# Kernel tuning notes

Hardware: AMD Instinct MI355X
Metric: run time of the kernel (lower is better)

The kernel has to match this reference:

```python
import jax, jax.numpy as jnp
import numpy as np

N, E, F_IN, H, C = 50000, 800000, 128, 4, 64
NEG_SLOPE = 0.2
LN_EPS = 1e-5


def setup_inputs() -> dict:
    key = jax.random.key(0)
    ks = jax.random.split(key, 8)
    s = 0.05
    return {
        "x": jax.random.normal(ks[0], (N, F_IN), jnp.float32),
        "edge_index": jax.random.randint(ks[1], (2, E), 0, N, jnp.int64).astype(jnp.int32),
        "Wl": jax.random.normal(ks[2], (F_IN, H * C), jnp.float32) * s,
        "bl": jnp.zeros((H * C,), jnp.float32),
        "Wr": jax.random.normal(ks[3], (F_IN, H * C), jnp.float32) * s,
        "br": jnp.zeros((H * C,), jnp.float32),
        "att": jax.random.normal(ks[4], (H, C), jnp.float32) * s,
        "bias_out": jnp.zeros((H * C,), jnp.float32),
        "Wproj": jax.random.normal(ks[5], (H * C, C), jnp.float32) * s,
        "ln_w": jnp.ones((C,), jnp.float32),
        "ln_b": jnp.zeros((C,), jnp.float32),
        "Wres": jax.random.normal(ks[6], (F_IN, C), jnp.float32) * s,
    }


def reference(x, edge_index, Wl, bl, Wr, br, att, bias_out, Wproj, ln_w, ln_b, Wres):
    n = x.shape[0]
    # add self loops (GATv2Conv add_self_loops=True)
    loop = jnp.arange(n, dtype=edge_index.dtype)
    src = jnp.concatenate([edge_index[0], loop])
    dst = jnp.concatenate([edge_index[1], loop])

    xl = (x @ Wl + bl).reshape(n, H, C)  # source-side transform
    xr = (x @ Wr + br).reshape(n, H, C)  # target-side transform

    # GATv2 edge scores: a^T LeakyReLU(xl_j + xr_i)
    m = xl[src] + xr[dst]                              # [Etot, H, C]
    e = jnp.einsum('ehc,hc->eh', jax.nn.leaky_relu(m, NEG_SLOPE), att)

    # segment softmax over incoming edges per destination node
    emax = jax.ops.segment_max(e, dst, num_segments=n)  # every node has a self loop
    ex = jnp.exp(e - emax[dst])
    denom = jax.ops.segment_sum(ex, dst, num_segments=n)
    alpha = ex / denom[dst]                             # [Etot, H]

    # scatter-aggregate messages, concat heads, output bias
    msg = xl[src] * alpha[:, :, None]                   # [Etot, H, C]
    out = jax.ops.segment_sum(msg, dst, num_segments=n).reshape(n, H * C) + bias_out

    # proj -> layernorm -> GELU -> (+ residual); dropout inactive in eval
    out = out @ Wproj                                   # [N, C]
    mu = out.mean(-1, keepdims=True)
    var = jnp.mean(jnp.square(out - mu), -1, keepdims=True)
    out = (out - mu) * jax.lax.rsqrt(var + LN_EPS) * ln_w + ln_b
    out = jax.nn.gelu(out, approximate=False)
    return out + x @ Wres
```

## Files before the change

### kernel.cpp

```cpp
#include <hip/hip_runtime.h>
#include <math.h>

#define NEG_SLOPE 0.2f
#define LN_EPS 1e-5f
#define HC 256
#define NHEAD 4
#define CDIM 64
#define FIN 128
#define CAP 96

typedef short bf16x8 __attribute__((ext_vector_type(8)));
typedef float f32x4  __attribute__((ext_vector_type(4)));

__device__ inline unsigned short f2bf(float f) {
    unsigned u = __builtin_bit_cast(unsigned, f);
    return (unsigned short)((u + 0x7FFFu + ((u >> 16) & 1u)) >> 16);
}
__device__ inline float bf2f(unsigned short s) {
    return __builtin_bit_cast(float, (unsigned)s << 16);
}
__device__ inline void unpack8(const uint4 u, float* f) {
    f[0] = __builtin_bit_cast(float, u.x << 16);
    f[1] = __builtin_bit_cast(float, u.x & 0xffff0000u);
    f[2] = __builtin_bit_cast(float, u.y << 16);
    f[3] = __builtin_bit_cast(float, u.y & 0xffff0000u);
    f[4] = __builtin_bit_cast(float, u.z << 16);
    f[5] = __builtin_bit_cast(float, u.z & 0xffff0000u);
    f[6] = __builtin_bit_cast(float, u.w << 16);
    f[7] = __builtin_bit_cast(float, u.w & 0xffff0000u);
}

__global__ __launch_bounds__(256) void k_setup(
    const float* __restrict__ x,
    const float* __restrict__ Wl, const float* __restrict__ Wr,
    const float* __restrict__ Wproj, const float* __restrict__ Wres,
    const float* __restrict__ bias_out, const float* __restrict__ att,
    const int* __restrict__ ei,
    ushort* __restrict__ xb,
    ushort* __restrict__ wlb, ushort* __restrict__ wrb,
    ushort* __restrict__ wpj, ushort* __restrict__ wrs,
    float* __restrict__ bpj, float* __restrict__ att_s,
    int* __restrict__ cnt, int* __restrict__ bucket,
    int nb_sc, int nb_cvt, int E, int n_nodes)
{
    const int t = threadIdx.x;
    const int b = blockIdx.x;

    if (b < nb_sc) {
        const int gid = b * 256 + t;
        if (gid < E) {
            const int s = ei[gid];
            const int d = ei[E + gid];
            const int slot = atomicAdd(&cnt[d], 1);
            __builtin_nontemporal_store(s, &bucket[d * CAP + slot]);
        }
    } else if (b < nb_sc + nb_cvt) {
        const long i = ((long)(b - nb_sc) * 256 + t) * 4;
        const float4 v = *reinterpret_cast<const float4*>(&x[i]);
        ushort4 o;
        o.x = f2bf(v.x); o.y = f2bf(v.y); o.z = f2bf(v.z); o.w = f2bf(v.w);
        *reinterpret_cast<ushort4*>(&xb[i]) = o;
    } else if (b < nb_sc + nb_cvt + 224) {
        const int gid = (b - nb_sc - nb_cvt) * 256 + t;
        if (gid < 32768) {
            const int idx = gid;
            const int j = idx & 7, n = (idx >> 3) & 255, q = idx >> 11;
            const int k = (q >> 2) * 32 + (q & 3) * 8 + j;
            wlb[idx] = f2bf(Wl[k * HC + n]);
            wrb[idx] = f2bf(Wr[k * HC + n]);
        } else if (gid < 49152) {
            const int idx = gid - 32768;
            const int j = idx & 7, n = (idx >> 3) & 63, q = idx >> 9;
            const int k = (q >> 2) * 32 + (q & 3) * 8 + j;
            wpj[idx] = f2bf(Wproj[k * CDIM + n]);
        } else {
            const int idx = gid - 49152;
            const int j = idx & 7, n = (idx >> 3) & 63, q = idx >> 9;
            const int k = (q >> 2) * 32 + (q & 3) * 8 + j;
            wrs[idx] = f2bf(Wres[k * CDIM + n]);
        }
    } else {
        att_s[t] = att[t] * 1.44269504088896f;
        __shared__ float part[4][CDIM];
        const int col = t & 63, q = t >> 6;
        float s = 0.f;
        for (int k = q * 64; k < q * 64 + 64; ++k)
            s += bias_out[k] * Wproj[k * CDIM + col];
        part[q][col] = s;
        __syncthreads();
        if (q == 0)
            bpj[col] = part[0][col] + part[1][col] + part[2][col] + part[3][col];
    }
}

__global__ __launch_bounds__(256) void k_linear_mfma(
    const ushort* __restrict__ xb,
    const ushort* __restrict__ wlb, const ushort* __restrict__ wrb,
    const float* __restrict__ bl, const float* __restrict__ br,
    ushort* __restrict__ xl, ushort* __restrict__ xr, int n_nodes)
{
    const int wid = blockIdx.x * 4 + (threadIdx.x >> 6);
    const int lane = threadIdx.x & 63;
    const int ntiles = n_nodes >> 4;
    if (wid >= ntiles * 2) return;
    const int side = wid & 1;
    const int tile = wid >> 1;

    const ushort* __restrict__ wb   = side ? wrb : wlb;
    const float*  __restrict__ bias = side ? br : bl;
    ushort*       __restrict__ outp = side ? xr : xl;

    const int m  = lane & 15;
    const int kb = lane >> 4;
    const long arow = ((long)tile * 16 + m) * FIN;

    f32x4 acc[16];
#pragma unroll
    for (int f = 0; f < 16; ++f) acc[f] = (f32x4){0.f, 0.f, 0.f, 0.f};

    for (int ks = 0; ks < 4; ++ks) {
        const bf16x8 xf = *reinterpret_cast<const bf16x8*>(&xb[arow + ks * 32 + kb * 8]);
        const ushort* __restrict__ wq = wb + (size_t)((ks * 4 + kb) * HC) * 8;
#pragma unroll
        for (int f = 0; f < 16; ++f) {
            const bf16x8 wf = *reinterpret_cast<const bf16x8*>(&wq[(f * 16 + m) * 8]);
            acc[f] = __builtin_amdgcn_mfma_f32_16x16x32_bf16(wf, xf, acc[f], 0, 0, 0);
        }
    }
    const long obase = ((long)tile * 16 + m) * HC;
#pragma unroll
    for (int f = 0; f < 16; ++f) {
        const int ch = f * 16 + kb * 4;
        const float4 bi = *reinterpret_cast<const float4*>(&bias[ch]);
        ushort4 o;
        o.x = f2bf(acc[f][0] + bi.x);
        o.y = f2bf(acc[f][1] + bi.y);
        o.z = f2bf(acc[f][2] + bi.z);
        o.w = f2bf(acc[f][3] + bi.w);
        *reinterpret_cast<ushort4*>(&outp[obase + ch]) = o;
    }
}

__global__ __launch_bounds__(256) void k_gat_gather(
    const int* __restrict__ cnt, const int* __restrict__ bucket,
    const ushort* __restrict__ xl, const ushort* __restrict__ xr,
    const float* __restrict__ att_s,
    ushort* __restrict__ agg, int n_nodes)
{
    const int node = blockIdx.x * 4 + (threadIdx.x >> 6);
    const int lane = threadIdx.x & 63;
    if (node >= n_nodes) return;

    const int cn = cnt[node];
    const int half = lane >> 5;
    const unsigned ch = (unsigned)(lane & 31) * 8;

    float xrv[8], atv[8];
    unpack8(*reinterpret_cast<const uint4*>(&xr[(unsigned)node * HC + ch]), xrv);
    const float4 a0 = *reinterpret_cast<const float4*>(&att_s[ch]);
    const float4 a1 = *reinterpret_cast<const float4*>(&att_s[ch + 4]);
    atv[0] = a0.x; atv[1] = a0.y; atv[2] = a0.z; atv[3] = a0.w;
    atv[4] = a1.x; atv[5] = a1.y; atv[6] = a1.z; atv[7] = a1.w;

    float cs[8];
    unpack8(*reinterpret_cast<const uint4*>(&xl[(unsigned)node * HC + ch]), cs);
    float ps = 0.f;
#pragma unroll
    for (int j = 0; j < 8; ++j) {
        float m = cs[j] + xrv[j];
        m = fmaxf(m, NEG_SLOPE * m);
        ps += m * atv[j];
    }
    ps += __shfl_xor(ps, 1);
    ps += __shfl_xor(ps, 2);
    ps += __shfl_xor(ps, 4);
    float es;
    asm("v_exp_f32 %0, %1" : "=v"(es) : "v"(ps));
    es = (half == 0) ? es : 0.f;
    float den = es;
    float ac[8];
#pragma unroll
    for (int j = 0; j < 8; ++j) ac[j] = es * cs[j];

    if (cn > 0) {
        const int beg = node * CAP;
        const int end = beg + cn;
        const int last = end - 1;

        const int i0 = bucket[min(beg + half, last)];
        const int i1 = bucket[min(beg + 2 + half, last)];
        const int i2 = bucket[min(beg + 4 + half, last)];
        const int i3 = bucket[min(beg + 6 + half, last)];
        int ip = bucket[min(beg + 8 + half, last)];
        int iq = bucket[min(beg + 10 + half, last)];
        uint4 d0 = *reinterpret_cast<const uint4*>(&xl[((unsigned)i0 << 8) + ch]);
        uint4 d1 = *reinterpret_cast<const uint4*>(&xl[((unsigned)i1 << 8) + ch]);
        uint4 d2 = *reinterpret_cast<const uint4*>(&xl[((unsigned)i2 << 8) + ch]);
        uint4 d3 = *reinterpret_cast<const uint4*>(&xl[((unsigned)i3 << 8) + ch]);

        for (int k = beg; k < end; k += 2) {
            const uint4 cu = d0;
            d0 = d1; d1 = d2; d2 = d3;
            d3 = *reinterpret_cast<const uint4*>(&xl[((unsigned)ip << 8) + ch]);
            ip = iq;
            iq = bucket[min(k + 12 + half, last)];

            float c[8];
            unpack8(cu, c);
            float p = 0.f;
#pragma unroll
            for (int j = 0; j < 8; ++j) {
                float m = c[j] + xrv[j];
                m = fmaxf(m, NEG_SLOPE * m);
                p += m * atv[j];
            }
            p += __shfl_xor(p, 1);
            p += __shfl_xor(p, 2);
            p += __shfl_xor(p, 4);

            float e;
            asm("v_exp_f32 %0, %1" : "=v"(e) : "v"(p));
            e = (k + half < end) ? e : 0.f;
            den += e;
#pragma unroll
            for (int j = 0; j < 8; ++j) ac[j] += e * c[j];
        }
    }

    den += __shfl_xor(den, 32);
#pragma unroll
    for (int j = 0; j < 8; ++j) ac[j] += __shfl_xor(ac[j], 32);

    if (lane < 32) {
        const float inv = 1.f / den;
        uint4 o;
        o.x = ((unsigned)f2bf(ac[1] * inv) << 16) | f2bf(ac[0] * inv);
        o.y = ((unsigned)f2bf(ac[3] * inv) << 16) | f2bf(ac[2] * inv);
        o.z = ((unsigned)f2bf(ac[5] * inv) << 16) | f2bf(ac[4] * inv);
        o.w = ((unsigned)f2bf(ac[7] * inv) << 16) | f2bf(ac[6] * inv);
        *reinterpret_cast<uint4*>(&agg[(unsigned)node * HC + ch]) = o;
    }
}

__global__ __launch_bounds__(256) void k_post_mfma(
    const ushort* __restrict__ aggb, const ushort* __restrict__ xb,
    const ushort* __restrict__ wpj, const ushort* __restrict__ wrs,
    const float* __restrict__ bpj,
    const float* __restrict__ ln_w, const float* __restrict__ ln_b,
    float* __restrict__ out, int n_nodes)
{
    const int wid = blockIdx.x * 4 + (threadIdx.x >> 6);
    const int lane = threadIdx.x & 63;
    const int ntiles = n_nodes >> 4;
    if (wid >= ntiles) return;

    const int m  = lane & 15;
    const int kb = lane >> 4;
    const long node = (long)wid * 16 + m;
    const long gbase = node * HC;
    const long xbase = node * FIN;

    f32x4 ap[4], ar[4];
#pragma unroll
    for (int f = 0; f < 4; ++f) {
        ap[f] = (f32x4){0.f, 0.f, 0.f, 0.f};
        ar[f] = (f32x4){0.f, 0.f, 0.f, 0.f};
    }

    for (int ks = 0; ks < 8; ++ks) {
        const bf16x8 af = *reinterpret_cast<const bf16x8*>(&aggb[gbase + ks * 32 + kb * 8]);
        const ushort* __restrict__ wq = wpj + (size_t)((ks * 4 + kb) * CDIM) * 8;
#pragma unroll
        for (int f = 0; f < 4; ++f) {
            const bf16x8 wf = *reinterpret_cast<const bf16x8*>(&wq[(f * 16 + m) * 8]);
            ap[f] = __builtin_amdgcn_mfma_f32_16x16x32_bf16(wf, af, ap[f], 0, 0, 0);
        }
    }
    for (int ks = 0; ks < 4; ++ks) {
        const bf16x8 af = *reinterpret_cast<const bf16x8*>(&xb[xbase + ks * 32 + kb * 8]);
        const ushort* __restrict__ wq = wrs + (size_t)((ks * 4 + kb) * CDIM) * 8;
#pragma unroll
        for (int f = 0; f < 4; ++f) {
            const bf16x8 wf = *reinterpret_cast<const bf16x8*>(&wq[(f * 16 + m) * 8]);
            ar[f] = __builtin_amdgcn_mfma_f32_16x16x32_bf16(wf, af, ar[f], 0, 0, 0);
        }
    }

    float p[4][4];
#pragma unroll
    for (int f = 0; f < 4; ++f) {
        const float4 bp = *reinterpret_cast<const float4*>(&bpj[f * 16 + kb * 4]);
#pragma unroll
        for (int j = 0; j < 4; ++j) p[f][j] = ap[f][j] + ((const float*)&bp)[j];
    }

    float s1 = 0.f;
#pragma unroll
    for (int f = 0; f < 4; ++f)
#pragma unroll
        for (int j = 0; j < 4; ++j) s1 += p[f][j];
    s1 += __shfl_xor(s1, 16); s1 += __shfl_xor(s1, 32);
    const float mu = s1 * (1.f / 64.f);

    float s2 = 0.f;
#pragma unroll
    for (int f = 0; f < 4; ++f)
#pragma unroll
        for (int j = 0; j < 4; ++j) {
            const float d = p[f][j] - mu;
            s2 += d * d;
        }
    s2 += __shfl_xor(s2, 16); s2 += __shfl_xor(s2, 32);
    const float rs = rsqrtf(s2 * (1.f / 64.f) + LN_EPS);

#pragma unroll
    for (int f = 0; f < 4; ++f) {
        const int ch = f * 16 + kb * 4;
        const float4 lw = *reinterpret_cast<const float4*>(&ln_w[ch]);
        const float4 lb = *reinterpret_cast<const float4*>(&ln_b[ch]);
        float4 ov;
#pragma unroll
        for (int j = 0; j < 4; ++j) {
            const float v = (p[f][j] - mu) * rs * ((const float*)&lw)[j] + ((const float*)&lb)[j];
            const float g = 0.5f * v * (1.f + erff(v * 0.70710678118654752f));
            ((float*)&ov)[j] = g + ar[f][j];
        }
        *reinterpret_cast<float4*>(&out[node * CDIM + ch]) = ov;
    }
}

extern "C" void kernel_launch(void* const* d_in, const int* in_sizes, int n_in,
                              void* d_out, int out_size, void* d_ws, size_t ws_size,
                              hipStream_t stream)
{
    const float* x        = (const float*)d_in[0];
    const int*   ei       = (const int*)  d_in[1];
    const float* Wl       = (const float*)d_in[2];
    const float* bl       = (const float*)d_in[3];
    const float* Wr       = (const float*)d_in[4];
    const float* br       = (const float*)d_in[5];
    const float* att      = (const float*)d_in[6];
    const float* bias_out = (const float*)d_in[7];
    const float* Wproj    = (const float*)d_in[8];
    const float* ln_w     = (const float*)d_in[9];
    const float* ln_b     = (const float*)d_in[10];
    const float* Wres     = (const float*)d_in[11];
    float* out = (float*)d_out;

    const int N = in_sizes[0] / FIN;
    const int E = in_sizes[1] / 2;
    const int ntiles = N >> 4;

    ushort* us = (ushort*)d_ws;
    size_t uo = 0;
    ushort* xl_bf  = us + uo; uo += (size_t)N * HC;
    ushort* xr_bf  = us + uo; uo += (size_t)N * HC;
    ushort* agg_bf = us + uo; uo += (size_t)N * HC;
    ushort* x_bf   = us + uo; uo += (size_t)N * FIN;
    ushort* wlb    = us + uo; uo += 32768;
    ushort* wrb    = us + uo; uo += 32768;
    ushort* wpj    = us + uo; uo += 16384;
    ushort* wrs    = us + uo; uo += 8192;
    float* bpj   = (float*)(us + uo);
    float* att_s = bpj + CDIM;
    int* cnt    = (int*)(att_s + HC);
    int* bucket = cnt + N;

    hipMemsetAsync(cnt, 0, (size_t)N * sizeof(int), stream);

    const int nb_sc  = (E + 255) / 256;
    const int nb_cvt = (N * FIN / 4 + 255) / 256;
    k_setup<<<nb_sc + nb_cvt + 224 + 1, 256, 0, stream>>>(
        x, Wl, Wr, Wproj, Wres, bias_out, att, ei,
        x_bf, wlb, wrb, wpj, wrs, bpj, att_s, cnt, bucket,
        nb_sc, nb_cvt, E, N);

    k_linear_mfma<<<(2 * ntiles + 3) / 4, 256, 0, stream>>>(
        x_bf, wlb, wrb, bl, br, xl_bf, xr_bf, N);

    k_gat_gather<<<(N + 3) / 4, 256, 0, stream>>>(
        cnt, bucket, xl_bf, xr_bf, att_s, agg_bf, N);

    k_post_mfma<<<(ntiles + 3) / 4, 256, 0, stream>>>(
        agg_bf, x_bf, wpj, wrs, bpj, ln_w, ln_b, out, N);
}
```

Before: 252.8 us.

## Fuse edge bucketing and x conversion into linear MFMA kernel, pad counters

Splits setup into a small weight-prep kernel and a combined kernel that runs edge bucketing blocks alongside the linear MFMA blocks. The linear blocks now read fp32 x directly and convert it to bf16 in registers, with one side writing x_bf for the later post kernel. This removes the separate x conversion pass and one launch boundary. Per-node counters are padded to a 16-int stride to spread the atomics across cache lines, at the cost of a larger memset and more counter memory.

```diff
diff --git a/kernel.cpp b/kernel.cpp
--- a/kernel.cpp
+++ b/kernel.cpp
@@ -8,6 +8,7 @@
 #define CDIM 64
 #define FIN 128
 #define CAP 96
+#define CSTRIDE 16
 
 typedef short bf16x8 __attribute__((ext_vector_type(8)));
 typedef float f32x4  __attribute__((ext_vector_type(4)));
@@ -30,38 +31,18 @@
     f[7] = __builtin_bit_cast(float, u.w & 0xffff0000u);
 }
 
-__global__ __launch_bounds__(256) void k_setup(
-    const float* __restrict__ x,
+__global__ __launch_bounds__(256) void k_prep(
     const float* __restrict__ Wl, const float* __restrict__ Wr,
     const float* __restrict__ Wproj, const float* __restrict__ Wres,
     const float* __restrict__ bias_out, const float* __restrict__ att,
-    const int* __restrict__ ei,
-    ushort* __restrict__ xb,
     ushort* __restrict__ wlb, ushort* __restrict__ wrb,
     ushort* __restrict__ wpj, ushort* __restrict__ wrs,
-    float* __restrict__ bpj, float* __restrict__ att_s,
-    int* __restrict__ cnt, int* __restrict__ bucket,
-    int nb_sc, int nb_cvt, int E, int n_nodes)
+    float* __restrict__ bpj, float* __restrict__ att_s)
 {
     const int t = threadIdx.x;
     const int b = blockIdx.x;
-
-    if (b < nb_sc) {
+    if (b < 224) {
         const int gid = b * 256 + t;
-        if (gid < E) {
-            const int s = ei[gid];
-            const int d = ei[E + gid];
-            const int slot = atomicAdd(&cnt[d], 1);
-            __builtin_nontemporal_store(s, &bucket[d * CAP + slot]);
-        }
-    } else if (b < nb_sc + nb_cvt) {
-        const long i = ((long)(b - nb_sc) * 256 + t) * 4;
-        const float4 v = *reinterpret_cast<const float4*>(&x[i]);
-        ushort4 o;
-        o.x = f2bf(v.x); o.y = f2bf(v.y); o.z = f2bf(v.z); o.w = f2bf(v.w);
-        *reinterpret_cast<ushort4*>(&xb[i]) = o;
-    } else if (b < nb_sc + nb_cvt + 224) {
-        const int gid = (b - nb_sc - nb_cvt) * 256 + t;
         if (gid < 32768) {
             const int idx = gid;
             const int j = idx & 7, n = (idx >> 3) & 255, q = idx >> 11;
@@ -93,14 +74,31 @@
     }
 }
 
-__global__ __launch_bounds__(256) void k_linear_mfma(
-    const ushort* __restrict__ xb,
+__global__ __launch_bounds__(256) void k_main(
+    const int* __restrict__ ei,
+    int* __restrict__ cnt, int* __restrict__ bucket,
+    const float* __restrict__ x,
     const ushort* __restrict__ wlb, const ushort* __restrict__ wrb,
     const float* __restrict__ bl, const float* __restrict__ br,
-    ushort* __restrict__ xl, ushort* __restrict__ xr, int n_nodes)
-{
-    const int wid = blockIdx.x * 4 + (threadIdx.x >> 6);
-    const int lane = threadIdx.x & 63;
+    ushort* __restrict__ x_bf,
+    ushort* __restrict__ xl, ushort* __restrict__ xr,
+    int nb_sc, int E, int n_nodes)
+{
+    const int t = threadIdx.x;
+
+    if (blockIdx.x < nb_sc) {
+        const int gid = blockIdx.x * 256 + t;
+        if (gid < E) {
+            const int s = ei[gid];
+            const int d = ei[E + gid];
+            const int slot = atomicAdd(&cnt[d * CSTRIDE], 1);
+            __builtin_nontemporal_store(s, &bucket[d * CAP + slot]);
+        }
+        return;
+    }
+
+    const int wid = (blockIdx.x - nb_sc) * 4 + (t >> 6);
+    const int lane = t & 63;
     const int ntiles = n_nodes >> 4;
     if (wid >= ntiles * 2) return;
     const int side = wid & 1;
@@ -119,12 +117,21 @@
     for (int f = 0; f < 16; ++f) acc[f] = (f32x4){0.f, 0.f, 0.f, 0.f};
 
     for (int ks = 0; ks < 4; ++ks) {
-        const bf16x8 xf = *reinterpret_cast<const bf16x8*>(&xb[arow + ks * 32 + kb * 8]);
+        const float4 lo = *reinterpret_cast<const float4*>(&x[arow + ks * 32 + kb * 8]);
+        const float4 hi = *reinterpret_cast<const float4*>(&x[arow + ks * 32 + kb * 8 + 4]);
+        union { bf16x8 v; ushort u[8]; } xf;
+        xf.u[0] = f2bf(lo.x); xf.u[1] = f2bf(lo.y);
+        xf.u[2] = f2bf(lo.z); xf.u[3] = f2bf(lo.w);
+        xf.u[4] = f2bf(hi.x); xf.u[5] = f2bf(hi.y);
+        xf.u[6] = f2bf(hi.z); xf.u[7] = f2bf(hi.w);
+        if (side == 0)
+            *reinterpret_cast<bf16x8*>(&x_bf[arow + ks * 32 + kb * 8]) = xf.v;
+
         const ushort* __restrict__ wq = wb + (size_t)((ks * 4 + kb) * HC) * 8;
 #pragma unroll
         for (int f = 0; f < 16; ++f) {
             const bf16x8 wf = *reinterpret_cast<const bf16x8*>(&wq[(f * 16 + m) * 8]);
-            acc[f] = __builtin_amdgcn_mfma_f32_16x16x32_bf16(wf, xf, acc[f], 0, 0, 0);
+            acc[f] = __builtin_amdgcn_mfma_f32_16x16x32_bf16(wf, xf.v, acc[f], 0, 0, 0);
         }
     }
     const long obase = ((long)tile * 16 + m) * HC;
@@ -151,7 +158,7 @@
     const int lane = threadIdx.x & 63;
     if (node >= n_nodes) return;
 
-    const int cn = cnt[node];
+    const int cn = cnt[node * CSTRIDE];
     const int half = lane >> 5;
     const unsigned ch = (unsigned)(lane & 31) * 8;
 
@@ -364,19 +371,20 @@
     float* bpj   = (float*)(us + uo);
     float* att_s = bpj + CDIM;
     int* cnt    = (int*)(att_s + HC);
-    int* bucket = cnt + N;
-
-    hipMemsetAsync(cnt, 0, (size_t)N * sizeof(int), stream);
-
-    const int nb_sc  = (E + 255) / 256;
-    const int nb_cvt = (N * FIN / 4 + 255) / 256;
-    k_setup<<<nb_sc + nb_cvt + 224 + 1, 256, 0, stream>>>(
-        x, Wl, Wr, Wproj, Wres, bias_out, att, ei,
-        x_bf, wlb, wrb, wpj, wrs, bpj, att_s, cnt, bucket,
-        nb_sc, nb_cvt, E, N);
-
-    k_linear_mfma<<<(2 * ntiles + 3) / 4, 256, 0, stream>>>(
-        x_bf, wlb, wrb, bl, br, xl_bf, xr_bf, N);
+    int* bucket = cnt + (size_t)N * CSTRIDE;
+
+    hipMemsetAsync(cnt, 0, (size_t)N * CSTRIDE * sizeof(int), stream);
+
+    k_prep<<<225, 256, 0, stream>>>(Wl, Wr, Wproj, Wres, bias_out, att,
+                                    wlb, wrb, wpj, wrs, bpj, att_s);
+
+    {
+        const int nb_sc  = (E + 255) / 256;
+        const int nb_lin = (2 * ntiles + 3) / 4;
+        k_main<<<nb_sc + nb_lin, 256, 0, stream>>>(
+            ei, cnt, bucket, x, wlb, wrb, bl, br,
+            x_bf, xl_bf, xr_bf, nb_sc, E, N);
+    }
 
     k_gat_gather<<<(N + 3) / 4, 256, 0, stream>>>(
         cnt, bucket, xl_bf, xr_bf, att_s, agg_bf, N);
```

Measured after the change: 229.9 us. 9.1% less time.
